# Optimization experiments

Hardware: AMD Instinct MI355X
Metric: run time of the kernel (lower is better)

The kernel has to match this reference:

```python
import jax, jax.numpy as jnp
import numpy as np

B, T, D, H = 8, 4096, 128, 64


def setup_inputs() -> dict:
    key = jax.random.key(0)
    kx, kf, kg = jax.random.split(key, 3)
    X = jax.random.normal(kx, (B, T, D), dtype=jnp.float32)
    Wf = jax.random.normal(kf, (D, H), dtype=jnp.float32) * 0.05   # Conv1D k=1 weight
    Wg = jax.random.normal(kg, (3, D, H), dtype=jnp.float32) * 0.05  # Conv1D k=3 weight
    return {"X": X, "Wf": Wf, "Wg": Wg}


def reference(X, Wf, Wg):
    # f(X): pointwise conv == matmul over feature dim
    f = jnp.einsum('btd,dh->bth', X, Wf)
    # g(X): kernel-3 'same' conv, taps at offsets -1,0,+1
    Xp = jnp.pad(X, ((0, 0), (1, 1), (0, 0)))
    Tlen = X.shape[1]
    g = (jnp.einsum('btd,dh->bth', Xp[:, 0:Tlen], Wg[0])
         + jnp.einsum('btd,dh->bth', Xp[:, 1:Tlen + 1], Wg[1])
         + jnp.einsum('btd,dh->bth', Xp[:, 2:Tlen + 2], Wg[2]))
    # scores [B,T,T], scaled by sqrt(h)
    M = jnp.einsum('bth,bsh->bts', f, g) / jnp.sqrt(jnp.float32(H))
    w = jax.nn.softmax(M, axis=-1)
    # values are the raw input X
    return jnp.einsum('bts,bsd->btd', w, X)
```

## Files before the change

### kernel.cpp

```cpp
#include <hip/hip_runtime.h>
#include <hip/hip_bf16.h>

#define B_ 8
#define T_ 4096
#define D_ 128
#define H_ 64
#define SBLK 64
#define NT (T_ / SBLK)

typedef short bf16x8 __attribute__((ext_vector_type(8)));
typedef float f32x4 __attribute__((ext_vector_type(4)));
typedef float f32x16 __attribute__((ext_vector_type(16)));
typedef _Float16 h4 __attribute__((ext_vector_type(4)));

__device__ __forceinline__ unsigned short f2bf(float f) {
  unsigned int u = __float_as_uint(f);
  u += 0x7fffu + ((u >> 16) & 1u);
  return (unsigned short)(u >> 16);
}

__device__ __forceinline__ void async_copy16(const void* g, void* l) {
  __builtin_amdgcn_global_load_lds((const __attribute__((address_space(1))) void*)g,
                                   (__attribute__((address_space(3))) void*)l, 16, 0, 0);
}

#define OFF_XP  0u
#define SZ_XP   ((unsigned)(B_*(T_+2)*D_*2))
#define OFF_XT  (OFF_XP + SZ_XP)
#define SZ_XT   ((unsigned)(B_*D_*T_*2))
#define OFF_F   (OFF_XT + SZ_XT)
#define SZ_F    ((unsigned)(B_*T_*H_*2))
#define OFF_G   (OFF_F + SZ_F)
#define OFF_WFT (OFF_G + SZ_F)
#define SZ_WFT  ((unsigned)(H_*D_*2))
#define OFF_WGT (OFF_WFT + SZ_WFT)
#define SZ_WGT  ((unsigned)(3*H_*D_*2))
#define OFF_PH1 (OFF_WGT + SZ_WGT)
#define SZ_PH1  ((unsigned)(B_*T_*D_*2))
#define OFF_PL  (OFF_PH1 + SZ_PH1)

#define SLOT(r) (((((r) & 3) << 1) ^ (((r) >> 2) & 1) ^ (((((r) >> 3) ^ ((r) >> 4)) & 1) << 2)))

__global__ __launch_bounds__(256) void prep_x(const float* __restrict__ X,
                                              unsigned short* __restrict__ Xp,
                                              unsigned short* __restrict__ XT) {
  __shared__ unsigned short tile[64][129];
  const int b = blockIdx.x;
  const int t0 = blockIdx.y * 64;
  const int tid = threadIdx.x;
#pragma unroll
  for (int c = 0; c < 8; ++c) {
    int i4 = tid + c * 256;
    int row = i4 >> 5, col4 = i4 & 31;
    float4 v = ((const float4*)X)[(size_t)(b * T_ + t0 + row) * 32 + col4];
    ushort4 h;
    h.x = f2bf(v.x); h.y = f2bf(v.y); h.z = f2bf(v.z); h.w = f2bf(v.w);
    ((ushort4*)Xp)[(size_t)(b * (T_ + 2) + 1 + t0 + row) * 32 + col4] = h;
    tile[row][col4 * 4 + 0] = h.x;
    tile[row][col4 * 4 + 1] = h.y;
    tile[row][col4 * 4 + 2] = h.z;
    tile[row][col4 * 4 + 3] = h.w;
  }
  if (blockIdx.y == 0 && tid < 32) {
    ushort4 z = {0, 0, 0, 0};
    ((ushort4*)Xp)[(size_t)(b * (T_ + 2) + 0) * 32 + tid] = z;
    ((ushort4*)Xp)[(size_t)(b * (T_ + 2) + T_ + 1) * 32 + tid] = z;
  }
  __syncthreads();
#pragma unroll
  for (int c = 0; c < 8; ++c) {
    int o4 = tid + c * 256;
    int d = o4 >> 4, t4 = o4 & 15;
    ushort4 h;
    h.x = tile[t4 * 4 + 0][d];
    h.y = tile[t4 * 4 + 1][d];
    h.z = tile[t4 * 4 + 2][d];
    h.w = tile[t4 * 4 + 3][d];
    ((ushort4*)XT)[(size_t)(b * 128 + d) * (T_ / 4) + (t0 >> 2) + t4] = h;
  }
}

__global__ __launch_bounds__(256) void prep_w(const float* __restrict__ Wf,
                                              const float* __restrict__ Wg,
                                              unsigned short* __restrict__ WfT,
                                              unsigned short* __restrict__ WgT) {
  const float SC = 0.18033688011112042f;
  int idx = blockIdx.x * 256 + threadIdx.x;
  if (idx < H_ * D_) {
    int h = idx >> 7, d = idx & 127;
    WfT[idx] = f2bf(Wf[d * H_ + h] * SC);
  } else {
    int j = idx - H_ * D_;
    int tap = j >> 13, r = j & 8191;
    int h = r >> 7, d = r & 127;
    WgT[j] = f2bf(Wg[tap * (D_ * H_) + d * H_ + h]);
  }
}

__global__ __launch_bounds__(64) void fg_kernel(const unsigned short* __restrict__ Xp,
                                                const unsigned short* __restrict__ WfT,
                                                const unsigned short* __restrict__ WgT,
                                                unsigned short* __restrict__ F,
                                                unsigned short* __restrict__ G) {
  const int lane = threadIdx.x;
  const int rowbase = blockIdx.x * 32;
  const int b = rowbase >> 12, t0 = rowbase & (T_ - 1);
  const int l15 = lane & 15, lhi = lane >> 4;
  const f32x4 fz = {0.f, 0.f, 0.f, 0.f};
  f32x4 accF[2][4], accG[2][4];
#pragma unroll
  for (int mt = 0; mt < 2; ++mt)
#pragma unroll
    for (int nt = 0; nt < 4; ++nt) { accF[mt][nt] = fz; accG[mt][nt] = fz; }

#pragma unroll
  for (int kk = 0; kk < 4; ++kk) {
    const int k0 = kk * 32 + lhi * 8;
    bf16x8 a[3][2];
#pragma unroll
    for (int sh = 0; sh < 3; ++sh)
#pragma unroll
      for (int mt = 0; mt < 2; ++mt) {
        int r = b * (T_ + 2) + t0 + sh + mt * 16 + l15;
        a[sh][mt] = *(const bf16x8*)&Xp[(size_t)r * 128 + k0];
      }
#pragma unroll
    for (int nt = 0; nt < 4; ++nt) {
      int h = nt * 16 + l15;
      bf16x8 wf  = *(const bf16x8*)&WfT[h * 128 + k0];
      bf16x8 wg0 = *(const bf16x8*)&WgT[(0 * 64 + h) * 128 + k0];
      bf16x8 wg1 = *(const bf16x8*)&WgT[(1 * 64 + h) * 128 + k0];
      bf16x8 wg2 = *(const bf16x8*)&WgT[(2 * 64 + h) * 128 + k0];
#pragma unroll
      for (int mt = 0; mt < 2; ++mt) {
        accF[mt][nt] = __builtin_amdgcn_mfma_f32_16x16x32_bf16(a[1][mt], wf,  accF[mt][nt], 0, 0, 0);
        accG[mt][nt] = __builtin_amdgcn_mfma_f32_16x16x32_bf16(a[0][mt], wg0, accG[mt][nt], 0, 0, 0);
        accG[mt][nt] = __builtin_amdgcn_mfma_f32_16x16x32_bf16(a[1][mt], wg1, accG[mt][nt], 0, 0, 0);
        accG[mt][nt] = __builtin_amdgcn_mfma_f32_16x16x32_bf16(a[2][mt], wg2, accG[mt][nt], 0, 0, 0);
      }
    }
  }
#pragma unroll
  for (int mt = 0; mt < 2; ++mt)
#pragma unroll
    for (int nt = 0; nt < 4; ++nt)
#pragma unroll
      for (int r = 0; r < 4; ++r) {
        int t = t0 + mt * 16 + lhi * 4 + r;
        int h = nt * 16 + l15;
        size_t o = (size_t)(b * T_ + t) * 64 + h;
        F[o] = f2bf(accF[mt][nt][r]);
        G[o] = f2bf(accG[mt][nt][r]);
      }
}

__global__ __launch_bounds__(256, 3) void attn_kernel(const unsigned short* __restrict__ F,
                                                      const unsigned short* __restrict__ G,
                                                      const unsigned short* __restrict__ XT,
                                                      float* __restrict__ out,
                                                      _Float16* __restrict__ PH0,
                                                      _Float16* __restrict__ PH1,
                                                      float* __restrict__ PL) {
  __shared__ unsigned short klds[64 * 64];
  __shared__ unsigned short vlds[2][128 * 64];
  const int b = blockIdx.x;
  const int q0 = blockIdx.y * 128;
  const int z = blockIdx.z;
  const int t_begin = (z == 0) ? 0 : 22 + (z - 1) * 21;
  const int t_count = (z == 0) ? 22 : 21;
  const int tid = threadIdx.x;
  const int wave = tid >> 6, lane = tid & 63;
  const int l31 = lane & 31, hi = lane >> 5;
  const int qw = q0 + wave * 32;
  const int E = SLOT(l31) << 4;

  bf16x8 qf[4];
#pragma unroll
  for (int ks = 0; ks < 4; ++ks)
    qf[ks] = *(const bf16x8*)&F[(size_t)(b * T_ + qw + l31) * 64 + ks * 16 + hi * 8];

  f32x16 o_acc[4];
#pragma unroll
  for (int nt = 0; nt < 4; ++nt)
#pragma unroll
    for (int r = 0; r < 16; ++r) o_acc[nt][r] = 0.f;
  float lsum = 0.f;

  const int lo3 = lane >> 3, lc = lane & 7;

  auto stageK = [&](int gt) {
    const int s0n = gt * SBLK;
#pragma unroll
    for (int i = 0; i < 2; ++i) {
      int kchunk = wave * 2 + i;
      int s = kchunk * 8 + lo3;
      int cp = lc ^ ((lo3 & 3) << 1) ^ ((lo3 >> 2) & 1) ^ (((kchunk ^ (kchunk >> 1)) & 1) << 2);
      async_copy16(&G[(size_t)(b * T_ + s0n + s) * 64 + cp * 8],
                   (char*)&klds[0] + kchunk * 1024);
    }
  };
  auto stageV = [&](int buf, int gt) {
    const int s0n = gt * SBLK;
#pragma unroll
    for (int i = 0; i < 4; ++i) {
      int vchunk = wave * 4 + i;
      int d = vchunk * 8 + lo3;
      int cp = lc ^ ((lo3 & 3) << 1) ^ ((lo3 >> 2) & 1) ^ (((vchunk ^ (vchunk >> 1)) & 1) << 2);
      async_copy16(&XT[(size_t)(b * 128 + d) * T_ + s0n + cp * 8],
                   (char*)&vlds[buf][0] + vchunk * 1024);
    }
  };

  union PW { unsigned u[4]; bf16x8 v; };
  auto makePA = [&](const f32x16& S, bf16x8& paA, bf16x8& paB) {
    float p[16];
#pragma unroll
    for (int r = 0; r < 16; ++r) p[r] = __builtin_amdgcn_exp2f(S[r]);
    lsum += (((p[0] + p[1]) + (p[2] + p[3])) + ((p[4] + p[5]) + (p[6] + p[7])))
          + (((p[8] + p[9]) + (p[10] + p[11])) + ((p[12] + p[13]) + (p[14] + p[15])));
    unsigned w[4][2];
#pragma unroll
    for (int g = 0; g < 4; ++g)
#pragma unroll
      for (int u = 0; u < 2; ++u) {
        union { __hip_bfloat162 h2; unsigned uu; } cv;
        cv.h2 = __float22bfloat162_rn(make_float2(p[4 * g + 2 * u], p[4 * g + 2 * u + 1]));
        w[g][u] = cv.uu;
      }
    PW pwA, pwB;
#pragma unroll
    for (int u = 0; u < 2; ++u) {
      unsigned A = w[0][u], Bv = w[1][u];
      asm("v_permlane32_swap_b32 %0, %1" : "+v"(A), "+v"(Bv));
      pwA.u[u] = A; pwA.u[2 + u] = Bv;
    }
#pragma unroll
    for (int u = 0; u < 2; ++u) {
      unsigned A = w[2][u], Bv = w[3][u];
      asm("v_permlane32_swap_b32 %0, %1" : "+v"(A), "+v"(Bv));
      pwB.u[u] = A; pwB.u[2 + u] = Bv;
    }
    paA = pwA.v; paB = pwB.v;
  };

  stageK(t_begin);
  stageV(0, t_begin);
  __syncthreads();

  for (int tt = 0; tt < t_count; ++tt) {
    const int cur = tt & 1;
    char* kbase = (char*)klds;
    char* vbase = (char*)vlds[cur];
    bf16x8 pa0, pa1, pa2, pa3;

    __builtin_amdgcn_s_setprio(1);
    {
      f32x16 S0;
#pragma unroll
      for (int r = 0; r < 16; ++r) S0[r] = 0.f;
#pragma unroll
      for (int ks = 0; ks < 4; ++ks) {
        bf16x8 k0 = *(const bf16x8*)(kbase + ((0 * 32 + l31) * 128 + ((ks * 32 + hi * 16) ^ E)));
        S0 = __builtin_amdgcn_mfma_f32_32x32x16_bf16(k0, qf[ks], S0, 0, 0, 0);
      }
      makePA(S0, pa0, pa1);
    }
    {
      f32x16 S1;
#pragma unroll
      for (int r = 0; r < 16; ++r) S1[r] = 0.f;
#pragma unroll
      for (int ks = 0; ks < 4; ++ks) {
        bf16x8 k1 = *(const bf16x8*)(kbase + ((1 * 32 + l31) * 128 + ((ks * 32 + hi * 16) ^ E)));
        S1 = __builtin_amdgcn_mfma_f32_32x32x16_bf16(k1, qf[ks], S1, 0, 0, 0);
      }
      makePA(S1, pa2, pa3);
    }
    __builtin_amdgcn_s_setprio(0);
    __syncthreads();

    if (tt + 1 < t_count) {
      stageK(t_begin + tt + 1);
      stageV(cur ^ 1, t_begin + tt + 1);
    }

    __builtin_amdgcn_s_setprio(1);
#pragma unroll
    for (int nt = 0; nt < 4; ++nt) {
      bf16x8 vf0 = *(const bf16x8*)(vbase + ((nt * 32 + l31) * 128 + ((0 * 32 + hi * 16) ^ E)));
      bf16x8 vf1 = *(const bf16x8*)(vbase + ((nt * 32 + l31) * 128 + ((1 * 32 + hi * 16) ^ E)));
      bf16x8 vf2 = *(const bf16x8*)(vbase + ((nt * 32 + l31) * 128 + ((2 * 32 + hi * 16) ^ E)));
      bf16x8 vf3 = *(const bf16x8*)(vbase + ((nt * 32 + l31) * 128 + ((3 * 32 + hi * 16) ^ E)));
      o_acc[nt] = __builtin_amdgcn_mfma_f32_32x32x16_bf16(pa0, vf0, o_acc[nt], 0, 0, 0);
      o_acc[nt] = __builtin_amdgcn_mfma_f32_32x32x16_bf16(pa1, vf1, o_acc[nt], 0, 0, 0);
      o_acc[nt] = __builtin_amdgcn_mfma_f32_32x32x16_bf16(pa2, vf2, o_acc[nt], 0, 0, 0);
      o_acc[nt] = __builtin_amdgcn_mfma_f32_32x32x16_bf16(pa3, vf3, o_acc[nt], 0, 0, 0);
    }
    __builtin_amdgcn_s_setprio(0);
    __syncthreads();
  }

  if (z == 2) {
#pragma unroll
    for (int r = 0; r < 16; ++r) {
      int trow = qw + (r & 3) + 8 * (r >> 2) + 4 * hi;
#pragma unroll
      for (int nt = 0; nt < 4; ++nt)
        out[(size_t)(b * T_ + trow) * 128 + nt * 32 + l31] = o_acc[nt][r];
    }
  } else {
    _Float16* ph = z ? PH1 : PH0;
#pragma unroll
    for (int r = 0; r < 16; ++r) {
      int trow = qw + (r & 3) + 8 * (r >> 2) + 4 * hi;
#pragma unroll
      for (int nt = 0; nt < 4; ++nt)
        ph[(size_t)(b * T_ + trow) * 128 + nt * 32 + l31] = (_Float16)o_acc[nt][r];
    }
  }
  lsum += __shfl_xor(lsum, 32, 64);
  if (hi == 0)
    PL[z * (B_ * T_) + b * T_ + qw + l31] = lsum;
}

__global__ __launch_bounds__(256) void merge_kernel(const _Float16* __restrict__ PH0,
                                                    const _Float16* __restrict__ PH1,
                                                    const float* __restrict__ PL,
                                                    float* __restrict__ out) {
  int idx = blockIdx.x * 256 + threadIdx.x;
  int row = idx >> 5;
  float4 o = ((const float4*)out)[idx];
  h4 p0 = *(const h4*)&PH0[(size_t)idx * 4];
  h4 p1 = *(const h4*)&PH1[(size_t)idx * 4];
  float inv = 1.0f / (PL[row] + PL[B_ * T_ + row] + PL[2 * B_ * T_ + row]);
  float4 r;
  r.x = (o.x + (float)p0.x + (float)p1.x) * inv;
  r.y = (o.y + (float)p0.y + (float)p1.y) * inv;
  r.z = (o.z + (float)p0.z + (float)p1.z) * inv;
  r.w = (o.w + (float)p0.w + (float)p1.w) * inv;
  ((float4*)out)[idx] = r;
}

extern "C" void kernel_launch(void* const* d_in, const int* in_sizes, int n_in,
                              void* d_out, int out_size, void* d_ws, size_t ws_size,
                              hipStream_t stream) {
  (void)in_sizes; (void)n_in; (void)out_size; (void)ws_size;
  const float* X  = (const float*)d_in[0];
  const float* Wf = (const float*)d_in[1];
  const float* Wg = (const float*)d_in[2];
  float* out = (float*)d_out;
  char* ws = (char*)d_ws;
  unsigned short* Xp  = (unsigned short*)(ws + OFF_XP);
  unsigned short* XT  = (unsigned short*)(ws + OFF_XT);
  unsigned short* Fb  = (unsigned short*)(ws + OFF_F);
  unsigned short* Gb  = (unsigned short*)(ws + OFF_G);
  unsigned short* WfT = (unsigned short*)(ws + OFF_WFT);
  unsigned short* WgT = (unsigned short*)(ws + OFF_WGT);
  _Float16* PH0 = (_Float16*)(ws + OFF_XP);
  _Float16* PH1 = (_Float16*)(ws + OFF_PH1);
  float* PL  = (float*)(ws + OFF_PL);

  prep_x<<<dim3(B_, T_ / 64), 256, 0, stream>>>(X, Xp, XT);
  prep_w<<<(H_ * D_ * 4) / 256, 256, 0, stream>>>(Wf, Wg, WfT, WgT);
  fg_kernel<<<(B_ * T_) / 32, 64, 0, stream>>>(Xp, WfT, WgT, Fb, Gb);
  attn_kernel<<<dim3(B_, T_ / 128, 3), 256, 0, stream>>>(Fb, Gb, XT, out, PH0, PH1, PL);
  merge_kernel<<<(B_ * T_ * D_ / 4) / 256, 256, 0, stream>>>(PH0, PH1, PL, out);
}
```

Before: 95.63 us.

## Double query rows per wave and switch to 4-way key split

Each wave now handles 64 query rows (two 32-row sub-tiles), so every K and V fragment read from LDS feeds two MFMAs instead of one, halving LDS traffic per FLOP. The key range is split 4 ways (or 2 if workspace is small) instead of 3, adding a third fp16 partial buffer and extending the merge kernel to match. Occupancy drops from 3 to 2 blocks per CU because register use grows, and the extra partial buffer adds global write and merge traffic.

```diff
diff --git a/kernel.cpp b/kernel.cpp
--- a/kernel.cpp
+++ b/kernel.cpp
@@ -36,8 +36,11 @@
 #define OFF_WGT (OFF_WFT + SZ_WFT)
 #define SZ_WGT  ((unsigned)(3*H_*D_*2))
 #define OFF_PH1 (OFF_WGT + SZ_WGT)
-#define SZ_PH1  ((unsigned)(B_*T_*D_*2))
-#define OFF_PL  (OFF_PH1 + SZ_PH1)
+#define SZ_PH   ((unsigned)(B_*T_*D_*2))
+#define OFF_PL  (OFF_PH1 + SZ_PH)
+#define SZ_PL   ((unsigned)(4*B_*T_*4))
+#define OFF_PH2 (OFF_PL + SZ_PL)
+#define WS_NEED4 ((size_t)(OFF_PH2 + SZ_PH))
 
 #define SLOT(r) (((((r) & 3) << 1) ^ (((r) >> 2) & 1) ^ (((((r) >> 3) ^ ((r) >> 4)) & 1) << 2)))
 
@@ -154,37 +157,44 @@
       }
 }
 
-__global__ __launch_bounds__(256, 3) void attn_kernel(const unsigned short* __restrict__ F,
+__global__ __launch_bounds__(256, 2) void attn_kernel(const unsigned short* __restrict__ F,
                                                       const unsigned short* __restrict__ G,
                                                       const unsigned short* __restrict__ XT,
                                                       float* __restrict__ out,
                                                       _Float16* __restrict__ PH0,
                                                       _Float16* __restrict__ PH1,
-                                                      float* __restrict__ PL) {
+                                                      _Float16* __restrict__ PH2,
+                                                      float* __restrict__ PL,
+                                                      int nsplit) {
   __shared__ unsigned short klds[64 * 64];
   __shared__ unsigned short vlds[2][128 * 64];
   const int b = blockIdx.x;
-  const int q0 = blockIdx.y * 128;
+  const int q0 = blockIdx.y * 256;
   const int z = blockIdx.z;
-  const int t_begin = (z == 0) ? 0 : 22 + (z - 1) * 21;
-  const int t_count = (z == 0) ? 22 : 21;
+  const int nt2 = NT / nsplit;
+  const int t_begin = z * nt2;
+  const int t_count = nt2;
   const int tid = threadIdx.x;
   const int wave = tid >> 6, lane = tid & 63;
   const int l31 = lane & 31, hi = lane >> 5;
-  const int qw = q0 + wave * 32;
+  const int qw = q0 + wave * 64;
   const int E = SLOT(l31) << 4;
 
-  bf16x8 qf[4];
-#pragma unroll
-  for (int ks = 0; ks < 4; ++ks)
-    qf[ks] = *(const bf16x8*)&F[(size_t)(b * T_ + qw + l31) * 64 + ks * 16 + hi * 8];
-
-  f32x16 o_acc[4];
-#pragma unroll
-  for (int nt = 0; nt < 4; ++nt)
-#pragma unroll
-    for (int r = 0; r < 16; ++r) o_acc[nt][r] = 0.f;
-  float lsum = 0.f;
+  bf16x8 qf[2][4];
+#pragma unroll
+  for (int nq = 0; nq < 2; ++nq)
+#pragma unroll
+    for (int ks = 0; ks < 4; ++ks)
+      qf[nq][ks] = *(const bf16x8*)&F[(size_t)(b * T_ + qw + nq * 32 + l31) * 64 + ks * 16 + hi * 8];
+
+  f32x16 o_acc[2][4];
+#pragma unroll
+  for (int nq = 0; nq < 2; ++nq)
+#pragma unroll
+    for (int nt = 0; nt < 4; ++nt)
+#pragma unroll
+      for (int r = 0; r < 16; ++r) o_acc[nq][nt][r] = 0.f;
+  float lsum0 = 0.f, lsum1 = 0.f;
 
   const int lo3 = lane >> 3, lc = lane & 7;
 
@@ -212,12 +222,12 @@
   };
 
   union PW { unsigned u[4]; bf16x8 v; };
-  auto makePA = [&](const f32x16& S, bf16x8& paA, bf16x8& paB) {
+  auto makePA = [&](const f32x16& S, bf16x8& paA, bf16x8& paB, float& ls) {
     float p[16];
 #pragma unroll
     for (int r = 0; r < 16; ++r) p[r] = __builtin_amdgcn_exp2f(S[r]);
-    lsum += (((p[0] + p[1]) + (p[2] + p[3])) + ((p[4] + p[5]) + (p[6] + p[7])))
-          + (((p[8] + p[9]) + (p[10] + p[11])) + ((p[12] + p[13]) + (p[14] + p[15])));
+    ls += (((p[0] + p[1]) + (p[2] + p[3])) + ((p[4] + p[5]) + (p[6] + p[7])))
+        + (((p[8] + p[9]) + (p[10] + p[11])) + ((p[12] + p[13]) + (p[14] + p[15])));
     unsigned w[4][2];
 #pragma unroll
     for (int g = 0; g < 4; ++g)
@@ -251,30 +261,33 @@
     const int cur = tt & 1;
     char* kbase = (char*)klds;
     char* vbase = (char*)vlds[cur];
-    bf16x8 pa0, pa1, pa2, pa3;
+    bf16x8 pa[2][4];
 
     __builtin_amdgcn_s_setprio(1);
-    {
-      f32x16 S0;
-#pragma unroll
-      for (int r = 0; r < 16; ++r) S0[r] = 0.f;
-#pragma unroll
-      for (int ks = 0; ks < 4; ++ks) {
-        bf16x8 k0 = *(const bf16x8*)(kbase + ((0 * 32 + l31) * 128 + ((ks * 32 + hi * 16) ^ E)));
-        S0 = __builtin_amdgcn_mfma_f32_32x32x16_bf16(k0, qf[ks], S0, 0, 0, 0);
-      }
-      makePA(S0, pa0, pa1);
-    }
-    {
-      f32x16 S1;
-#pragma unroll
-      for (int r = 0; r < 16; ++r) S1[r] = 0.f;
-#pragma unroll
-      for (int ks = 0; ks < 4; ++ks) {
-        bf16x8 k1 = *(const bf16x8*)(kbase + ((1 * 32 + l31) * 128 + ((ks * 32 + hi * 16) ^ E)));
-        S1 = __builtin_amdgcn_mfma_f32_32x32x16_bf16(k1, qf[ks], S1, 0, 0, 0);
-      }
-      makePA(S1, pa2, pa3);
+#pragma unroll
+    for (int st = 0; st < 2; ++st) {
+      bf16x8 kf[4];
+#pragma unroll
+      for (int ks = 0; ks < 4; ++ks)
+        kf[ks] = *(const bf16x8*)(kbase + ((st * 32 + l31) * 128 + ((ks * 32 + hi * 16) ^ E)));
+      {
+        f32x16 S;
+#pragma unroll
+        for (int r = 0; r < 16; ++r) S[r] = 0.f;
+#pragma unroll
+        for (int ks = 0; ks < 4; ++ks)
+          S = __builtin_amdgcn_mfma_f32_32x32x16_bf16(kf[ks], qf[0][ks], S, 0, 0, 0);
+        makePA(S, pa[0][st * 2], pa[0][st * 2 + 1], lsum0);
+      }
+      {
+        f32x16 S;
+#pragma unroll
+        for (int r = 0; r < 16; ++r) S[r] = 0.f;
+#pragma unroll
+        for (int ks = 0; ks < 4; ++ks)
+          S = __builtin_amdgcn_mfma_f32_32x32x16_bf16(kf[ks], qf[1][ks], S, 0, 0, 0);
+        makePA(S, pa[1][st * 2], pa[1][st * 2 + 1], lsum1);
+      }
     }
     __builtin_amdgcn_s_setprio(0);
     __syncthreads();
@@ -287,64 +300,84 @@
     __builtin_amdgcn_s_setprio(1);
 #pragma unroll
     for (int nt = 0; nt < 4; ++nt) {
-      bf16x8 vf0 = *(const bf16x8*)(vbase + ((nt * 32 + l31) * 128 + ((0 * 32 + hi * 16) ^ E)));
-      bf16x8 vf1 = *(const bf16x8*)(vbase + ((nt * 32 + l31) * 128 + ((1 * 32 + hi * 16) ^ E)));
-      bf16x8 vf2 = *(const bf16x8*)(vbase + ((nt * 32 + l31) * 128 + ((2 * 32 + hi * 16) ^ E)));
-      bf16x8 vf3 = *(const bf16x8*)(vbase + ((nt * 32 + l31) * 128 + ((3 * 32 + hi * 16) ^ E)));
-      o_acc[nt] = __builtin_amdgcn_mfma_f32_32x32x16_bf16(pa0, vf0, o_acc[nt], 0, 0, 0);
-      o_acc[nt] = __builtin_amdgcn_mfma_f32_32x32x16_bf16(pa1, vf1, o_acc[nt], 0, 0, 0);
-      o_acc[nt] = __builtin_amdgcn_mfma_f32_32x32x16_bf16(pa2, vf2, o_acc[nt], 0, 0, 0);
-      o_acc[nt] = __builtin_amdgcn_mfma_f32_32x32x16_bf16(pa3, vf3, o_acc[nt], 0, 0, 0);
+      bf16x8 vf[4];
+#pragma unroll
+      for (int kk = 0; kk < 4; ++kk)
+        vf[kk] = *(const bf16x8*)(vbase + ((nt * 32 + l31) * 128 + ((kk * 32 + hi * 16) ^ E)));
+#pragma unroll
+      for (int kk = 0; kk < 4; ++kk) {
+        o_acc[0][nt] = __builtin_amdgcn_mfma_f32_32x32x16_bf16(pa[0][kk], vf[kk], o_acc[0][nt], 0, 0, 0);
+        o_acc[1][nt] = __builtin_amdgcn_mfma_f32_32x32x16_bf16(pa[1][kk], vf[kk], o_acc[1][nt], 0, 0, 0);
+      }
     }
     __builtin_amdgcn_s_setprio(0);
     __syncthreads();
   }
 
-  if (z == 2) {
-#pragma unroll
-    for (int r = 0; r < 16; ++r) {
-      int trow = qw + (r & 3) + 8 * (r >> 2) + 4 * hi;
-#pragma unroll
-      for (int nt = 0; nt < 4; ++nt)
-        out[(size_t)(b * T_ + trow) * 128 + nt * 32 + l31] = o_acc[nt][r];
-    }
+  if (z == nsplit - 1) {
+#pragma unroll
+    for (int nq = 0; nq < 2; ++nq)
+#pragma unroll
+      for (int r = 0; r < 16; ++r) {
+        int trow = qw + nq * 32 + (r & 3) + 8 * (r >> 2) + 4 * hi;
+#pragma unroll
+        for (int nt = 0; nt < 4; ++nt)
+          out[(size_t)(b * T_ + trow) * 128 + nt * 32 + l31] = o_acc[nq][nt][r];
+      }
   } else {
-    _Float16* ph = z ? PH1 : PH0;
-#pragma unroll
-    for (int r = 0; r < 16; ++r) {
-      int trow = qw + (r & 3) + 8 * (r >> 2) + 4 * hi;
-#pragma unroll
-      for (int nt = 0; nt < 4; ++nt)
-        ph[(size_t)(b * T_ + trow) * 128 + nt * 32 + l31] = (_Float16)o_acc[nt][r];
-    }
-  }
-  lsum += __shfl_xor(lsum, 32, 64);
-  if (hi == 0)
-    PL[z * (B_ * T_) + b * T_ + qw + l31] = lsum;
+    _Float16* ph = (z == 0) ? PH0 : (z == 1) ? PH1 : PH2;
+#pragma unroll
+    for (int nq = 0; nq < 2; ++nq)
+#pragma unroll
+      for (int r = 0; r < 16; ++r) {
+        int trow = qw + nq * 32 + (r & 3) + 8 * (r >> 2) + 4 * hi;
+#pragma unroll
+        for (int nt = 0; nt < 4; ++nt)
+          ph[(size_t)(b * T_ + trow) * 128 + nt * 32 + l31] = (_Float16)o_acc[nq][nt][r];
+      }
+  }
+  lsum0 += __shfl_xor(lsum0, 32, 64);
+  lsum1 += __shfl_xor(lsum1, 32, 64);
+  if (hi == 0) {
+    PL[z * (B_ * T_) + b * T_ + qw + l31] = lsum0;
+    PL[z * (B_ * T_) + b * T_ + qw + 32 + l31] = lsum1;
+  }
 }
 
 __global__ __launch_bounds__(256) void merge_kernel(const _Float16* __restrict__ PH0,
                                                     const _Float16* __restrict__ PH1,
+                                                    const _Float16* __restrict__ PH2,
                                                     const float* __restrict__ PL,
-                                                    float* __restrict__ out) {
+                                                    float* __restrict__ out,
+                                                    int nsplit) {
   int idx = blockIdx.x * 256 + threadIdx.x;
   int row = idx >> 5;
   float4 o = ((const float4*)out)[idx];
   h4 p0 = *(const h4*)&PH0[(size_t)idx * 4];
-  h4 p1 = *(const h4*)&PH1[(size_t)idx * 4];
-  float inv = 1.0f / (PL[row] + PL[B_ * T_ + row] + PL[2 * B_ * T_ + row]);
+  float den = PL[row] + PL[B_ * T_ + row];
+  float ax = (float)p0.x, ay = (float)p0.y, az = (float)p0.z, aw = (float)p0.w;
+  if (nsplit == 4) {
+    h4 p1 = *(const h4*)&PH1[(size_t)idx * 4];
+    h4 p2 = *(const h4*)&PH2[(size_t)idx * 4];
+    ax += (float)p1.x + (float)p2.x;
+    ay += (float)p1.y + (float)p2.y;
+    az += (float)p1.z + (float)p2.z;
+    aw += (float)p1.w + (float)p2.w;
+    den += PL[2 * B_ * T_ + row] + PL[3 * B_ * T_ + row];
+  }
+  float inv = 1.0f / den;
   float4 r;
-  r.x = (o.x + (float)p0.x + (float)p1.x) * inv;
-  r.y = (o.y + (float)p0.y + (float)p1.y) * inv;
-  r.z = (o.z + (float)p0.z + (float)p1.z) * inv;
-  r.w = (o.w + (float)p0.w + (float)p1.w) * inv;
+  r.x = (o.x + ax) * inv;
+  r.y = (o.y + ay) * inv;
+  r.z = (o.z + az) * inv;
+  r.w = (o.w + aw) * inv;
   ((float4*)out)[idx] = r;
 }
 
 extern "C" void kernel_launch(void* const* d_in, const int* in_sizes, int n_in,
                               void* d_out, int out_size, void* d_ws, size_t ws_size,
                               hipStream_t stream) {
-  (void)in_sizes; (void)n_in; (void)out_size; (void)ws_size;
+  (void)in_sizes; (void)n_in; (void)out_size;
   const float* X  = (const float*)d_in[0];
   const float* Wf = (const float*)d_in[1];
   const float* Wg = (const float*)d_in[2];
@@ -358,11 +391,15 @@
   unsigned short* WgT = (unsigned short*)(ws + OFF_WGT);
   _Float16* PH0 = (_Float16*)(ws + OFF_XP);
   _Float16* PH1 = (_Float16*)(ws + OFF_PH1);
+  _Float16* PH2 = (_Float16*)(ws + OFF_PH2);
   float* PL  = (float*)(ws + OFF_PL);
+
+  const int nsplit = (ws_size >= WS_NEED4) ? 4 : 2;
 
   prep_x<<<dim3(B_, T_ / 64), 256, 0, stream>>>(X, Xp, XT);
   prep_w<<<(H_ * D_ * 4) / 256, 256, 0, stream>>>(Wf, Wg, WfT, WgT);
   fg_kernel<<<(B_ * T_) / 32, 64, 0, stream>>>(Xp, WfT, WgT, Fb, Gb);
-  attn_kernel<<<dim3(B_, T_ / 128, 3), 256, 0, stream>>>(Fb, Gb, XT, out, PH0, PH1, PL);
-  merge_kernel<<<(B_ * T_ * D_ / 4) / 256, 256, 0, stream>>>(PH0, PH1, PL, out);
-}
+  attn_kernel<<<dim3(B_, T_ / 256, nsplit), 256, 0, stream>>>(Fb, Gb, XT, out,
+                                                              PH0, PH1, PH2, PL, nsplit);
+  merge_kernel<<<(B_ * T_ * D_ / 4) / 256, 256, 0, stream>>>(PH0, PH1, PH2, PL, out, nsplit);
+}
```

Result: slower. 185.6 us (+94.1%).
